# Kernel optimization log

Hardware: AMD Instinct MI355X
Metric: run time of the kernel (lower is better)

Reference implementation:

```python
import math
import jax, jax.numpy as jnp
from jax import lax
import numpy as np

B, TX, TY, NF = 32, 512, 2048, 80
LOG2PI = math.log(2.0 * math.pi)
NEG = -1e9


def sequence_mask(lengths, maxlen):
    return jnp.arange(maxlen)[None, :] < lengths[:, None]


def maximum_path(lp, mask, x_lengths, y_lengths):
    """Monotonic alignment search (Viterbi DP) over a [B,TX,TY] log-prior grid.
    Equivalent to monotonic_align.maximum_path (Cython kernel in Matcha-TTS)."""
    b, tx, ty = lp.shape
    lp = jnp.where(mask, lp, NEG)
    lp_t = jnp.moveaxis(lp, 2, 0)  # [TY, B, TX] - scan over mel time
    i = jnp.arange(tx)
    # j = 0: path must start at text position 0
    v0 = jnp.where(i[None, :] == 0, lp_t[0], NEG)  # [B, TX]

    def fwd(v, lp_j):
        v_shift = jnp.concatenate([jnp.full((b, 1), NEG, v.dtype), v[:, :-1]], axis=1)
        from_diag = v_shift >= v  # came from (i-1, j-1)? ties -> diagonal (matches Cython >=)
        v_new = lp_j + jnp.maximum(v, v_shift)
        return v_new, from_diag

    _, dirs = lax.scan(fwd, v0, lp_t[1:])  # [TY-1, B, TX] bool
    dirs = jnp.concatenate([jnp.zeros((1, b, tx), bool), dirs], axis=0)  # [TY, B, TX]

    # Backtrack from (x_len-1, y_len-1) down to (0, 0).
    idx0 = (x_lengths - 1).astype(jnp.int32)

    def bwd(idx, inp):
        j, dir_j = inp
        active = j < y_lengths  # [B]
        row = (i[None, :] == idx[:, None]) & active[:, None]  # one-hot path row at time j
        move = jnp.take_along_axis(dir_j, idx[:, None].astype(jnp.int32), axis=1)[:, 0]
        idx_new = jnp.where(active, idx - move.astype(idx.dtype), idx)
        return idx_new, row

    js = jnp.arange(ty - 1, -1, -1)
    _, rows = lax.scan(bwd, idx0, (js, dirs[::-1]))  # rows in reverse-j order
    path = jnp.moveaxis(rows[::-1], 0, 2)  # [B, TX, TY]
    return path.astype(lp.dtype)


def setup_inputs() -> dict:
    key = jax.random.key(0)
    k = jax.random.split(key, 5)
    mu_x = jax.random.normal(k[0], (B, NF, TX), jnp.float32)
    logw = jax.random.normal(k[1], (B, 1, TX), jnp.float32) * 0.5
    y = jax.random.normal(k[2], (B, NF, TY), jnp.float32)
    x_lengths = jax.random.randint(k[3], (B,), TX // 2, TX + 1)
    y_lengths = jax.random.randint(k[4], (B,), TY // 2, TY + 1)
    return {"mu_x": mu_x, "logw": logw, "y": y,
            "x_lengths": x_lengths, "y_lengths": y_lengths}


def reference(mu_x, logw, y, x_lengths, y_lengths):
    x_mask = sequence_mask(x_lengths, TX)[:, None, :].astype(mu_x.dtype)  # [B,1,TX]
    y_mask = sequence_mask(y_lengths, TY)[:, None, :].astype(mu_x.dtype)  # [B,1,TY]
    logw = logw * x_mask  # encoder emits masked log-durations
    attn_mask = (x_mask[:, 0, :, None] * y_mask[:, 0, None, :]) > 0  # [B,TX,TY]

    # Gaussian log-prior: const - 0.5*y^2 + mu*y - 0.5*mu^2, summed over n_feats
    const = -0.5 * LOG2PI * NF
    y_square = -0.5 * jnp.sum(y * y, axis=1)[:, None, :]          # [B,1,TY]
    y_mu = jnp.einsum('bcx,bcy->bxy', mu_x, y)                    # [B,TX,TY]
    mu_square = -0.5 * jnp.sum(mu_x * mu_x, axis=1)[:, :, None]   # [B,TX,1]
    log_prior = y_square + y_mu + mu_square + const

    attn = maximum_path(log_prior, attn_mask, x_lengths, y_lengths)  # [B,TX,TY]

    # duration loss (MSE in log-duration space, normalized by total text length)
    logw_ = jnp.log(1e-8 + jnp.sum(attn, axis=-1))[:, None, :] * x_mask
    dur_loss = jnp.sum((logw - logw_) ** 2) / jnp.sum(x_lengths).astype(mu_x.dtype)

    # expand encoder means along the alignment
    mu_y = jnp.einsum('bxy,bcx->bcy', attn, mu_x)  # [B,NF,TY]

    prior_loss = jnp.sum(0.5 * ((y - mu_y) ** 2 + LOG2PI) * y_mask)
    prior_loss = prior_loss / (jnp.sum(y_mask) * NF)
    return dur_loss, prior_loss, attn
```

## Files before the change

### kernel.cpp

```cpp
#include <hip/hip_runtime.h>
#include <math.h>

#define B_  32
#define TX_ 512
#define TY_ 2048
#define NF_ 80
#define NEGF (-1e9f)

typedef unsigned long long u64;
typedef const __attribute__((address_space(1))) void* gas_t;
typedef __attribute__((address_space(3))) void* las_t;
typedef float f32x4 __attribute__((ext_vector_type(4)));

static constexpr float LOG2PI_F = 1.8378770664093453f;
static constexpr float CONST_F = (float)(-0.5 * 1.8378770664093454966 * 80.0);

__device__ inline float block_reduce_sum(float v) {
    __shared__ float sred[8];
    const int lane = threadIdx.x & 63, w = threadIdx.x >> 6;
    #pragma unroll
    for (int o = 32; o; o >>= 1) v += __shfl_down(v, o);
    if (lane == 0) sred[w] = v;
    __syncthreads();
    float r = 0.f;
    if (threadIdx.x == 0) {
        const int nw = blockDim.x >> 6;
        for (int k = 0; k < nw; ++k) r += sred[k];
    }
    return r;
}

__global__ __launch_bounds__(256) void sq_kernel(
    const float* __restrict__ mu, const float* __restrict__ yy,
    float* __restrict__ musq, float* __restrict__ ysq)
{
    const int t = blockIdx.x * 256 + threadIdx.x;
    const int nY = B_ * TY_;
    if (t < nY) {
        const int b = t >> 11, j = t & (TY_ - 1);
        const float* p = yy + (size_t)b * NF_ * TY_ + j;
        float s = 0.f;
        #pragma unroll 8
        for (int k = 0; k < NF_; ++k) { float v = p[(size_t)k * TY_]; s = fmaf(v, v, s); }
        ysq[t] = -0.5f * s;
    } else {
        const int t2 = t - nY;
        if (t2 < B_ * TX_) {
            const int b = t2 >> 9, i = t2 & (TX_ - 1);
            const float* p = mu + (size_t)b * NF_ * TX_ + i;
            float s = 0.f;
            #pragma unroll 8
            for (int k = 0; k < NF_; ++k) { float v = p[(size_t)k * TX_]; s = fmaf(v, v, s); }
            musq[t2] = -0.5f * s;
        }
    }
}

__global__ __launch_bounds__(256) void lp_kernel(
    const float* __restrict__ mu, const float* __restrict__ yy,
    const float* __restrict__ musq, const float* __restrict__ ysq,
    const int* __restrict__ xl, const int* __restrict__ yl,
    float* __restrict__ lp)
{
    __shared__ float smu[NF_][64];
    __shared__ float sy[NF_][64];
    const int b  = blockIdx.z;
    const int j0 = blockIdx.y * 64;
    const int ylen = yl[b];
    if (j0 >= ylen) return;
    const int i0 = blockIdx.x * 64;
    const int tid = threadIdx.x;

    const float* mub = mu + (size_t)b * NF_ * TX_ + i0;
    const float* yb  = yy + (size_t)b * NF_ * TY_ + j0;
    for (int t = tid; t < NF_ * 64; t += 256) {
        const int k = t >> 6, c = t & 63;
        smu[k][c] = mub[(size_t)k * TX_ + c];
        sy[k][c]  = yb[(size_t)k * TY_ + c];
    }
    __syncthreads();

    const int tx = tid & 15, ty = tid >> 4;
    float acc[4][4] = {};
    #pragma unroll 8
    for (int k = 0; k < NF_; ++k) {
        const float4 av = *(const float4*)&smu[k][tx * 4];
        const float4 bv = *(const float4*)&sy[k][ty * 4];
        const float a[4]  = {av.x, av.y, av.z, av.w};
        const float bb[4] = {bv.x, bv.y, bv.z, bv.w};
        #pragma unroll
        for (int r = 0; r < 4; ++r)
            #pragma unroll
            for (int c = 0; c < 4; ++c)
                acc[r][c] = fmaf(bb[r], a[c], acc[r][c]);
    }

    const int xlen = xl[b];
    float mq[4];
    #pragma unroll
    for (int c = 0; c < 4; ++c) mq[c] = musq[b * TX_ + i0 + tx * 4 + c];

    #pragma unroll
    for (int r = 0; r < 4; ++r) {
        const int j = j0 + ty * 4 + r;
        const float base = ysq[b * TY_ + j] + CONST_F;
        float4 o;
        float* po = &o.x;
        #pragma unroll
        for (int c = 0; c < 4; ++c) {
            const int i = i0 + tx * 4 + c;
            const float val = acc[r][c] + base + mq[c];
            po[c] = (i < xlen && j < ylen) ? val : NEGF;
        }
        *(float4*)&lp[((size_t)b * TY_ + j) * TX_ + i0 + tx * 4] = o;
    }
}

__global__ __launch_bounds__(64) void dp_kernel(
    const float* __restrict__ lp, const int* __restrict__ xl, const int* __restrict__ yl,
    int* __restrict__ idx_out, int* __restrict__ dur_out)
{
    extern __shared__ unsigned char smem[];
    unsigned char* dirs = smem;
    float* ring = (float*)(smem + 131072);
    int*   durs = (int*)(smem + 131072 + 24576);
    u64*   stg  = (u64*)(smem + 131072 + 24576 + 2048);

    const int b = blockIdx.x;
    const int lane = threadIdx.x;
    const int xlen = xl[b], ylen = yl[b];
    const int last = ylen - 1;

    #pragma unroll
    for (int u = 0; u < TX_ / 64; ++u) durs[lane + u * 64] = 0;
    dirs[lane] = 0;

    const float* lprow = lp + (size_t)b * TY_ * TX_;

    float v[8];
    #pragma unroll
    for (int u = 0; u < 8; ++u) v[u] = NEGF;
    if (lane == 0) v[0] = lprow[0];

    const unsigned ring_base = (unsigned)(uintptr_t)(las_t)ring;
    const unsigned dirs_base = (unsigned)(uintptr_t)(las_t)dirs;
    const int bpaddr = (lane - 1) * 4;

    auto stage_row = [&](int row, int slot) {
        const float* src = lprow + (size_t)row * TX_ + lane * 4;
        float* dst = ring + slot * TX_;
        __builtin_amdgcn_global_load_lds((gas_t)src,         (las_t)dst,         16, 0, 0);
        __builtin_amdgcn_global_load_lds((gas_t)(src + 256), (las_t)(dst + 256), 16, 0, 0);
    };

    auto step = [&](int j, int slot) {
        const unsigned laddr = ring_base + (unsigned)(slot * (TX_ * 4) + lane * 32);
        f32x4 lo, hi;
        float left;
        asm volatile(
            "s_waitcnt vmcnt(22)\n\t"
            "ds_read_b128 %0, %3\n\t"
            "ds_read_b128 %1, %3 offset:16\n\t"
            "ds_bpermute_b32 %2, %4, %5\n\t"
            "s_waitcnt lgkmcnt(0)"
            : "=&v"(lo), "=&v"(hi), "=&v"(left)
            : "v"(laddr), "v"(bpaddr), "v"(v[7]));
        const float lv[8] = {lo.x, lo.y, lo.z, lo.w, hi.x, hi.y, hi.z, hi.w};
        unsigned bits = 0u;
        float nv[8];
        #pragma unroll
        for (int u2 = 7; u2 >= 1; --u2) {
            const float p = v[u2 - 1];
            if (p >= v[u2]) bits |= (1u << u2);
            nv[u2] = lv[u2] + fmaxf(v[u2], p);
        }
        if (lane == 0) left = NEGF;
        if (left >= v[0]) bits |= 1u;
        nv[0] = lv[0] + fmaxf(v[0], left);
        #pragma unroll
        for (int u2 = 0; u2 < 8; ++u2) v[u2] = nv[u2];
        const unsigned daddr = dirs_base + (unsigned)(j * 64 + lane);
        asm volatile("ds_write_b8 %0, %1" :: "v"(daddr), "v"(bits));
    };

    auto renorm = [&]() {
        const float m = __int_as_float(__builtin_amdgcn_readfirstlane(__float_as_int(v[0])));
        #pragma unroll
        for (int u = 0; u < 8; ++u) v[u] -= m;
    };

    #pragma unroll
    for (int u = 0; u < 11; ++u) stage_row(1 + u, u);

    int r = 1, s = 0;
    while (r + 11 <= last) {
        stage_row(r + 11, (s == 0) ? 11 : s - 1);
        __builtin_amdgcn_sched_barrier(0);
        step(r, s);
        if ((r & 31) == 0) renorm();
        ++r; s = (s + 1 == 12) ? 0 : s + 1;
    }
    asm volatile("s_waitcnt vmcnt(0)");
    for (; r <= last; ++r) {
        step(r, s);
        s = (s + 1 == 12) ? 0 : s + 1;
    }

    asm volatile("s_waitcnt lgkmcnt(0)");
    __builtin_amdgcn_sched_barrier(0);
    __syncthreads();

    int* iout = idx_out + b * TY_;
    for (int jj = ylen + lane; jj < TY_; jj += 64) iout[jj] = -1;

    int idx = xlen - 1;
    int cnt = 0;
    int j0 = last;
    while (j0 >= 0) {
        const int n = (j0 + 1 < 56) ? (j0 + 1) : 56;
        const int A = min(max((idx >> 6) - 1, 0), 6) * 64;
        if (lane < n) {
            const unsigned char* rp = &dirs[(j0 - lane) * 64 + (A >> 3)];
            stg[lane * 2]     = *(const u64*)rp;
            stg[lane * 2 + 1] = *(const u64*)(rp + 8);
        }
        __syncthreads();
        for (int u = 0; u < n; ++u) {
            if (lane == 0) iout[j0 - u] = idx;
            const int sh = idx - A;
            const u64 w = (sh < 64) ? stg[u * 2] : stg[u * 2 + 1];
            const int bit = (int)((w >> (sh & 63)) & 1ULL);
            ++cnt;
            if (bit) { if (lane == 0) durs[idx] = cnt; cnt = 0; --idx; }
        }
        j0 -= n;
        __syncthreads();
    }
    if (lane == 0) durs[idx] = cnt;
    __syncthreads();

    #pragma unroll
    for (int u = 0; u < TX_ / 64; ++u)
        dur_out[b * TX_ + lane + u * 64] = durs[lane + u * 64];
}

__global__ __launch_bounds__(256) void attn_kernel(
    const int* __restrict__ idxs, float* __restrict__ attn )
{
    const int i = blockIdx.x;
    const int b = blockIdx.y;
    const int t = threadIdx.x;
    const int4* ib = (const int4*)(idxs + b * TY_);
    float* ob = attn + ((size_t)b * TX_ + i) * TY_ + t * 8;
    const int4 q0 = ib[t * 2];
    const int4 q1 = ib[t * 2 + 1];
    ((float2*)ob)[0] = make_float2(q0.x == i ? 1.f : 0.f, q0.y == i ? 1.f : 0.f);
    ((float2*)ob)[1] = make_float2(q0.z == i ? 1.f : 0.f, q0.w == i ? 1.f : 0.f);
    ((float2*)ob)[2] = make_float2(q1.x == i ? 1.f : 0.f, q1.y == i ? 1.f : 0.f);
    ((float2*)ob)[3] = make_float2(q1.z == i ? 1.f : 0.f, q1.w == i ? 1.f : 0.f);
}

__global__ __launch_bounds__(512) void dloss_kernel(
    const float* __restrict__ logw, const int* __restrict__ dur,
    const int* __restrict__ xl, double* __restrict__ acc)
{
    const int b = blockIdx.x;
    const int i = threadIdx.x;
    float s = 0.f;
    if (i < xl[b]) {
        const float lw  = logw[b * TX_ + i];
        const float lw_ = logf(1e-8f + (float)dur[b * TX_ + i]);
        const float d = lw - lw_;
        s = d * d;
    }
    const float r = block_reduce_sum(s);
    if (threadIdx.x == 0) atomicAdd(acc + 0, (double)r);
}

__global__ __launch_bounds__(256) void ploss_kernel(
    const float* __restrict__ mu, const float* __restrict__ yy,
    const int* __restrict__ idxs, const int* __restrict__ yl,
    double* __restrict__ acc)
{
    const int b = blockIdx.y;
    const int j = blockIdx.x * 256 + threadIdx.x;
    float s = 0.f;
    if (j < yl[b]) {
        const int ii = idxs[b * TY_ + j];
        const float* yp = yy + (size_t)b * NF_ * TY_ + j;
        const float* mp = mu + (size_t)b * NF_ * TX_ + ii;
        float sq = 0.f;
        #pragma unroll 8
        for (int k = 0; k < NF_; ++k) {
            const float d = yp[(size_t)k * TY_] - mp[(size_t)k * TX_];
            sq = fmaf(d, d, sq);
        }
        s = 0.5f * (sq + (float)NF_ * LOG2PI_F);
    }
    const float r = block_reduce_sum(s);
    if (threadIdx.x == 0) atomicAdd(acc + 1, (double)r);
}

__global__ void fin_kernel(const double* __restrict__ acc,
                           const int* __restrict__ xl, const int* __restrict__ yl,
                           float* __restrict__ out)
{
    if (threadIdx.x == 0 && blockIdx.x == 0) {
        long long sx = 0, sy = 0;
        for (int b = 0; b < B_; ++b) { sx += xl[b]; sy += yl[b]; }
        out[0] = (float)(acc[0] / (double)sx);
        out[1] = (float)(acc[1] / ((double)sy * (double)NF_));
    }
}

extern "C" void kernel_launch(void* const* d_in, const int* in_sizes, int n_in,
                              void* d_out, int out_size, void* d_ws, size_t ws_size,
                              hipStream_t stream)
{
    const float* mu   = (const float*)d_in[0];
    const float* logw = (const float*)d_in[1];
    const float* yy   = (const float*)d_in[2];
    const int*   xl   = (const int*)d_in[3];
    const int*   yl   = (const int*)d_in[4];
    float* out = (float*)d_out;

    char* ws = (char*)d_ws;
    float*  ysq  = (float*)(ws);
    float*  musq = (float*)(ws + 262144);
    int*    idxs = (int*)  (ws + 327680);
    int*    dur  = (int*)  (ws + 589824);
    double* acc  = (double*)(ws + 655360);

    float* lpbuf = out;
    float* attn  = out + 2;

    const size_t dp_lds = 131072 + 24576 + 2048 + 896;

    hipMemsetAsync(acc, 0, 16, stream);
    sq_kernel<<<dim3((B_ * (TY_ + TX_) + 255) / 256), 256, 0, stream>>>(mu, yy, musq, ysq);
    lp_kernel<<<dim3(TX_ / 64, TY_ / 64, B_), 256, 0, stream>>>(mu, yy, musq, ysq, xl, yl, lpbuf);
    dp_kernel<<<dim3(B_), 64, dp_lds, stream>>>(lpbuf, xl, yl, idxs, dur);
    attn_kernel<<<dim3(TX_, B_), 256, 0, stream>>>(idxs, attn);
    dloss_kernel<<<dim3(B_), 512, 0, stream>>>(logw, dur, xl, acc);
    ploss_kernel<<<dim3(TY_ / 256, B_), 256, 0, stream>>>(mu, yy, idxs, yl, acc);
    fin_kernel<<<1, 64, 0, stream>>>(acc, xl, yl, out);
}
```

Baseline: 772.2 us.

## Software-pipeline DP LDS row loads and use DPP shift instead of bpermute

Restructures the serial Viterbi DP loop so the LDS read of the next row is issued before computing the current row, with a double-buffered register pair and a two-row unrolled loop. The ring buffer grows from 12 to 14 slots for deeper global prefetch, and the cross-lane neighbour fetch moves from ds_bpermute to a DPP wave_shr move that stays out of LDS. Renormalisation now happens every 32 rows, once per 16 two-row iterations. This shortens the per-step latency chain in the single-wave DP. The cost is more LDS use and fragile hand-tuned waitcnt counts.

```diff
diff --git a/kernel.cpp b/kernel.cpp
--- a/kernel.cpp
+++ b/kernel.cpp
@@ -123,8 +123,8 @@
     extern __shared__ unsigned char smem[];
     unsigned char* dirs = smem;
     float* ring = (float*)(smem + 131072);
-    int*   durs = (int*)(smem + 131072 + 24576);
-    u64*   stg  = (u64*)(smem + 131072 + 24576 + 2048);
+    int*   durs = (int*)(smem + 131072 + 28672);
+    u64*   stg  = (u64*)(smem + 131072 + 28672 + 2048);
 
     const int b = blockIdx.x;
     const int lane = threadIdx.x;
@@ -141,10 +141,10 @@
     #pragma unroll
     for (int u = 0; u < 8; ++u) v[u] = NEGF;
     if (lane == 0) v[0] = lprow[0];
+    asm volatile("" : "+v"(v[0]));
 
     const unsigned ring_base = (unsigned)(uintptr_t)(las_t)ring;
     const unsigned dirs_base = (unsigned)(uintptr_t)(las_t)dirs;
-    const int bpaddr = (lane - 1) * 4;
 
     auto stage_row = [&](int row, int slot) {
         const float* src = lprow + (size_t)row * TX_ + lane * 4;
@@ -153,18 +153,19 @@
         __builtin_amdgcn_global_load_lds((gas_t)(src + 256), (las_t)(dst + 256), 16, 0, 0);
     };
 
-    auto step = [&](int j, int slot) {
-        const unsigned laddr = ring_base + (unsigned)(slot * (TX_ * 4) + lane * 32);
-        f32x4 lo, hi;
+    auto ld_row = [&](int slot, f32x4& lo, f32x4& hi) {
+        const unsigned laddr = ring_base + (unsigned)(slot * (TX_ * 4)) + (unsigned)(lane * 32);
+        asm volatile("ds_read_b128 %0, %2\n\t"
+                     "ds_read_b128 %1, %2 offset:16"
+                     : "=&v"(lo), "=&v"(hi) : "v"(laddr));
+    };
+
+    auto row_compute = [&](int j, const f32x4& lo, const f32x4& hi) {
         float left;
-        asm volatile(
-            "s_waitcnt vmcnt(22)\n\t"
-            "ds_read_b128 %0, %3\n\t"
-            "ds_read_b128 %1, %3 offset:16\n\t"
-            "ds_bpermute_b32 %2, %4, %5\n\t"
-            "s_waitcnt lgkmcnt(0)"
-            : "=&v"(lo), "=&v"(hi), "=&v"(left)
-            : "v"(laddr), "v"(bpaddr), "v"(v[7]));
+        asm volatile("s_nop 1\n\t"
+                     "v_mov_b32_dpp %0, %1 wave_shr:1 row_mask:0xf bank_mask:0xf"
+                     : "=&v"(left) : "v"(v[7]));
+        if (lane == 0) left = NEGF;
         const float lv[8] = {lo.x, lo.y, lo.z, lo.w, hi.x, hi.y, hi.z, hi.w};
         unsigned bits = 0u;
         float nv[8];
@@ -174,12 +175,11 @@
             if (p >= v[u2]) bits |= (1u << u2);
             nv[u2] = lv[u2] + fmaxf(v[u2], p);
         }
-        if (lane == 0) left = NEGF;
         if (left >= v[0]) bits |= 1u;
         nv[0] = lv[0] + fmaxf(v[0], left);
         #pragma unroll
         for (int u2 = 0; u2 < 8; ++u2) v[u2] = nv[u2];
-        const unsigned daddr = dirs_base + (unsigned)(j * 64 + lane);
+        const unsigned daddr = dirs_base + (unsigned)(j * 64) + (unsigned)lane;
         asm volatile("ds_write_b8 %0, %1" :: "v"(daddr), "v"(bits));
     };
 
@@ -189,24 +189,53 @@
         for (int u = 0; u < 8; ++u) v[u] -= m;
     };
 
-    #pragma unroll
-    for (int u = 0; u < 11; ++u) stage_row(1 + u, u);
-
-    int r = 1, s = 0;
-    while (r + 11 <= last) {
-        stage_row(r + 11, (s == 0) ? 11 : s - 1);
+    auto slotof = [&](int j) { int s = (j - 1) % 14; return s; };
+
+    f32x4 Alo, Ahi, Blo, Bhi;
+
+    #pragma unroll
+    for (int u = 0; u < 13; ++u) stage_row(1 + u, u);
+    asm volatile("s_waitcnt vmcnt(24)" ::: "memory");
+    ld_row(0, Alo, Ahi);
+    asm volatile("s_waitcnt lgkmcnt(0)" ::: "memory");
+    __builtin_amdgcn_sched_barrier(0);
+
+    int r = 1, g = 0;
+    while (r + 14 <= last) {
+        stage_row(r + 13, slotof(r + 13));
+        asm volatile("s_waitcnt vmcnt(24)" ::: "memory");
+        ld_row(slotof(r + 1), Blo, Bhi);
+        row_compute(r, Alo, Ahi);
+        asm volatile("s_waitcnt lgkmcnt(0)" ::: "memory");
         __builtin_amdgcn_sched_barrier(0);
-        step(r, s);
-        if ((r & 31) == 0) renorm();
-        ++r; s = (s + 1 == 12) ? 0 : s + 1;
-    }
-    asm volatile("s_waitcnt vmcnt(0)");
-    for (; r <= last; ++r) {
-        step(r, s);
-        s = (s + 1 == 12) ? 0 : s + 1;
-    }
-
-    asm volatile("s_waitcnt lgkmcnt(0)");
+
+        stage_row(r + 14, slotof(r + 14));
+        asm volatile("s_waitcnt vmcnt(24)" ::: "memory");
+        ld_row(slotof(r + 2), Alo, Ahi);
+        row_compute(r + 1, Blo, Bhi);
+        asm volatile("s_waitcnt lgkmcnt(0)" ::: "memory");
+        __builtin_amdgcn_sched_barrier(0);
+
+        if (((++g) & 15) == 0) renorm();
+        r += 2;
+    }
+
+    if (r + 13 <= last) stage_row(r + 13, slotof(r + 13));
+    asm volatile("s_waitcnt vmcnt(0)" ::: "memory");
+    while (r + 1 <= last) {
+        ld_row(slotof(r + 1), Blo, Bhi);
+        row_compute(r, Alo, Ahi);
+        asm volatile("s_waitcnt lgkmcnt(0)" ::: "memory");
+        __builtin_amdgcn_sched_barrier(0);
+        if (r + 2 <= last) ld_row(slotof(r + 2), Alo, Ahi);
+        row_compute(r + 1, Blo, Bhi);
+        asm volatile("s_waitcnt lgkmcnt(0)" ::: "memory");
+        __builtin_amdgcn_sched_barrier(0);
+        r += 2;
+    }
+    if (r == last) row_compute(r, Alo, Ahi);
+
+    asm volatile("s_waitcnt lgkmcnt(0)" ::: "memory");
     __builtin_amdgcn_sched_barrier(0);
     __syncthreads();
 
@@ -334,7 +363,7 @@
     float* lpbuf = out;
     float* attn  = out + 2;
 
-    const size_t dp_lds = 131072 + 24576 + 2048 + 896;
+    const size_t dp_lds = 131072 + 28672 + 2048 + 896;
 
     hipMemsetAsync(acc, 0, 16, stream);
     sq_kernel<<<dim3((B_ * (TY_ + TX_) + 255) / 256), 256, 0, stream>>>(mu, yy, musq, ysq);
```

After: 790.0 us. 1.02x slower.
